# Kernel tuning notes

Measured on AMD Instinct MI355X. Metric: run time of the kernel, lower is better.

The kernel has to match this reference:

```python
import jax, jax.numpy as jnp
import numpy as np

C = 512
NUM_HEADS = 8
HEAD_DIM = C // NUM_HEADS


def setup_inputs() -> dict:
    key = jax.random.key(0)
    ks = jax.random.split(key, 5)
    B, H, W = 4, 48, 48
    x = jax.random.normal(ks[0], (B, C, H, W), dtype=jnp.float32)
    # 1x1 conv weights == dense matrices over channel dim
    Wqkv = jax.random.normal(ks[1], (3 * C, C), dtype=jnp.float32) * (1.0 / np.sqrt(C))
    bqkv = jax.random.normal(ks[2], (3 * C,), dtype=jnp.float32) * 0.01
    Wout = jax.random.normal(ks[3], (C, C), dtype=jnp.float32) * (1.0 / np.sqrt(C))
    bout = jax.random.normal(ks[4], (C,), dtype=jnp.float32) * 0.01
    return {"x": x, "Wqkv": Wqkv, "bqkv": bqkv, "Wout": Wout, "bout": bout}


def reference(x, Wqkv, bqkv, Wout, bout):
    B, Cc, H, W = x.shape
    S = H * W
    # qkv 1x1 conv: [B, 3C, H, W] -> reshape (B, 3, heads, head_dim, S)
    qkv = jnp.einsum('bchw,oc->bohw', x, Wqkv) + bqkv[None, :, None, None]
    qkv = qkv.reshape(B, 3, NUM_HEADS, HEAD_DIM, S)
    q, k, v = qkv[:, 0], qkv[:, 1], qkv[:, 2]  # [B, h, d, S]
    # tokens along S: q^T k, scaled softmax
    scale = HEAD_DIM ** -0.5
    attn = jnp.einsum('bhds,bhdt->bhst', q, k) * scale  # [B, h, S, S]
    attn = jax.nn.softmax(attn, axis=-1)
    out = jnp.einsum('bhst,bhdt->bhds', attn, v)  # [B, h, d, S]
    out = out.reshape(B, Cc, H, W)
    out = jnp.einsum('bchw,oc->bohw', out, Wout) + bout[None, :, None, None]
    return out
```

## Files before the change

kernel.cpp:

```cpp
#include <hip/hip_runtime.h>

#define S_LEN 2304
#define CDIM  512
#define NHEAD 8

typedef __attribute__((ext_vector_type(4)))  float f32x4;
typedef __attribute__((ext_vector_type(16))) float f32x16;
typedef __attribute__((ext_vector_type(8)))  _Float16 f16x8;
typedef __attribute__((ext_vector_type(2)))  __fp16 fp16x2r;
typedef _Float16 h16;

#define QSCALE 0.18033688011112042f

__device__ __forceinline__ float fexp2(float x) {
#if __has_builtin(__builtin_amdgcn_exp2f)
    return __builtin_amdgcn_exp2f(x);
#else
    return exp2f(x);
#endif
}

__device__ __forceinline__ unsigned cvtpk(float a, float b) {
    union { fp16x2r v; unsigned u; } c;
    c.v = __builtin_amdgcn_cvt_pkrtz(a, b);
    return c.u;
}

__device__ __forceinline__ void gll16(const h16* g, h16* l) {
    __builtin_amdgcn_global_load_lds(
        (const __attribute__((address_space(1))) unsigned int*)g,
        (__attribute__((address_space(3))) unsigned int*)l, 16, 0, 0);
}

__global__ __launch_bounds__(256) void xpose_x(
    const float* __restrict__ x, h16* __restrict__ xT)
{
    const int s0 = blockIdx.x * 64;
    const int c0 = blockIdx.y * 64;
    const int b  = blockIdx.z;
    __shared__ h16 Ts[64][76];

    const int t  = threadIdx.x;
    const int cq = t >> 4;
    const int sq = t & 15;

    const float* xb = x + ((size_t)b * CDIM + c0 + cq * 4) * S_LEN + s0 + sq * 4;
    float4 r0 = *(const float4*)(xb);
    float4 r1 = *(const float4*)(xb + S_LEN);
    float4 r2 = *(const float4*)(xb + 2 * S_LEN);
    float4 r3 = *(const float4*)(xb + 3 * S_LEN);

    union { h16 h[4]; uint2 u; } pk;
    pk.h[0]=(h16)r0.x; pk.h[1]=(h16)r1.x; pk.h[2]=(h16)r2.x; pk.h[3]=(h16)r3.x;
    *(uint2*)&Ts[sq*4+0][cq*4] = pk.u;
    pk.h[0]=(h16)r0.y; pk.h[1]=(h16)r1.y; pk.h[2]=(h16)r2.y; pk.h[3]=(h16)r3.y;
    *(uint2*)&Ts[sq*4+1][cq*4] = pk.u;
    pk.h[0]=(h16)r0.z; pk.h[1]=(h16)r1.z; pk.h[2]=(h16)r2.z; pk.h[3]=(h16)r3.z;
    *(uint2*)&Ts[sq*4+2][cq*4] = pk.u;
    pk.h[0]=(h16)r0.w; pk.h[1]=(h16)r1.w; pk.h[2]=(h16)r2.w; pk.h[3]=(h16)r3.w;
    *(uint2*)&Ts[sq*4+3][cq*4] = pk.u;

    __syncthreads();
    const int s  = t >> 2;
    const int cc = (t & 3) * 16;
    uint2 a0 = *(uint2*)&Ts[s][cc + 0];
    uint2 a1 = *(uint2*)&Ts[s][cc + 4];
    uint2 a2 = *(uint2*)&Ts[s][cc + 8];
    uint2 a3 = *(uint2*)&Ts[s][cc + 12];
    h16* dst = xT + ((size_t)b * S_LEN + s0 + s) * CDIM + c0 + cc;
    uint4 w0 = make_uint4(a0.x, a0.y, a1.x, a1.y);
    uint4 w1 = make_uint4(a2.x, a2.y, a3.x, a3.y);
    *(uint4*)dst       = w0;
    *(uint4*)(dst + 8) = w1;
}

__global__ __launch_bounds__(256) void wconv(
    const float* __restrict__ Wq, const float* __restrict__ Wo,
    h16* __restrict__ Wq_h, h16* __restrict__ Wo_h)
{
    const int NQ = 1536 * 512;
    const int NO = 512 * 512;
    int i = (blockIdx.x * 256 + threadIdx.x) * 4;
    if (i >= NQ + NO) return;
    float4 v;
    h16* dst;
    if (i < NQ) { v = *(const float4*)(Wq + i);        dst = Wq_h + i; }
    else        { v = *(const float4*)(Wo + (i - NQ)); dst = Wo_h + (i - NQ); }
    union { h16 h[4]; uint2 u; } pk;
    pk.h[0]=(h16)v.x; pk.h[1]=(h16)v.y; pk.h[2]=(h16)v.z; pk.h[3]=(h16)v.w;
    *(uint2*)dst = pk.u;
}

__global__ __launch_bounds__(256) void gemm_qkv(
    const h16* __restrict__ Wh, const float* __restrict__ bqkv,
    const h16* __restrict__ xT, h16* __restrict__ qT, h16* __restrict__ kT,
    h16* __restrict__ vN)
{
    const int n0 = blockIdx.x * 128;
    const int m0 = blockIdx.y * 128;
    const int b  = blockIdx.z;
    __shared__ h16 Ws[128 * 64];
    __shared__ h16 Xs[128 * 64];

    const int tid = threadIdx.x;
    const int lid = tid & 63, w = tid >> 6;
    const int g = lid >> 4, ln = lid & 15;
    const int wm = w & 1, wn = w >> 1;
    const int srow = lid >> 3;
    const int sblk = (lid & 7) ^ (srow & 7);

    f32x4 acc[4][4];
#pragma unroll
    for (int i = 0; i < 4; i++)
#pragma unroll
        for (int j = 0; j < 4; j++) acc[i][j] = (f32x4)0.f;

    const h16* Wbase = Wh + (size_t)m0 * CDIM;
    const h16* Xbase = xT + ((size_t)b * S_LEN + n0) * CDIM;
    const bool vblk = (m0 >= 1024);

    for (int kt = 0; kt < CDIM; kt += 64) {
        __syncthreads();
#pragma unroll
        for (int i = 0; i < 4; i++) {
            const int row0 = w * 32 + i * 8;
            gll16(Wbase + (size_t)(row0 + srow) * CDIM + kt + sblk * 8, &Ws[row0 * 64]);
            gll16(Xbase + (size_t)(row0 + srow) * CDIM + kt + sblk * 8, &Xs[row0 * 64]);
        }
        __syncthreads();

#pragma unroll
        for (int kc = 0; kc < 2; kc++) {
            f16x8 af[4], bf[4];
#pragma unroll
            for (int i = 0; i < 4; i++) {
                const int ra = wm * 64 + i * 16 + ln;
                const int ca = (kc * 64 + g * 16) ^ ((ra & 7) << 4);
                af[i] = *(const f16x8*)&Ws[ra * 64 + ca / 2];
                const int rb = wn * 64 + i * 16 + ln;
                const int cb = (kc * 64 + g * 16) ^ ((rb & 7) << 4);
                bf[i] = *(const f16x8*)&Xs[rb * 64 + cb / 2];
            }
            if (!vblk) {
#pragma unroll
                for (int i = 0; i < 4; i++)
#pragma unroll
                    for (int j = 0; j < 4; j++)
                        acc[i][j] = __builtin_amdgcn_mfma_f32_16x16x32_f16(
                            af[i], bf[j], acc[i][j], 0, 0, 0);
            } else {
#pragma unroll
                for (int i = 0; i < 4; i++)
#pragma unroll
                    for (int j = 0; j < 4; j++)
                        acc[i][j] = __builtin_amdgcn_mfma_f32_16x16x32_f16(
                            bf[i], af[j], acc[i][j], 0, 0, 0);
            }
        }
    }

    if (!vblk) {
#pragma unroll
        for (int i = 0; i < 4; i++) {
            const int mb = m0 + wm * 64 + i * 16 + 4 * g;
            const float4 bv = *(const float4*)&bqkv[mb];
            const int mloc = mb & 511;
            const int hh = mloc >> 6, d0 = mloc & 63;
            const bool isq = (mb < 512);
            const float scl = isq ? QSCALE : 1.0f;
            h16* base = (isq ? qT : kT);
#pragma unroll
            for (int j = 0; j < 4; j++) {
                const int n = n0 + wn * 64 + j * 16 + ln;
                union { h16 h[4]; uint2 u; } pk;
                pk.h[0] = (h16)((acc[i][j][0] + bv.x) * scl);
                pk.h[1] = (h16)((acc[i][j][1] + bv.y) * scl);
                pk.h[2] = (h16)((acc[i][j][2] + bv.z) * scl);
                pk.h[3] = (h16)((acc[i][j][3] + bv.w) * scl);
                *(uint2*)(base + (((size_t)b * 8 + hh) * S_LEN + n) * 64 + d0) = pk.u;
            }
        }
    } else {
#pragma unroll
        for (int j = 0; j < 4; j++) {
            const int m = m0 + wm * 64 + j * 16 + ln;
            const float bias = bqkv[m];
            const int mloc = m - 1024;
            const int hh = mloc >> 6, d = mloc & 63;
            h16* base = vN + (((size_t)b * 8 + hh) * 64 + d) * S_LEN;
#pragma unroll
            for (int i = 0; i < 4; i++) {
                const int nb = n0 + wn * 64 + i * 16 + 4 * g;
                union { h16 h[4]; uint2 u; } pk;
                pk.h[0] = (h16)(acc[i][j][0] + bias);
                pk.h[1] = (h16)(acc[i][j][1] + bias);
                pk.h[2] = (h16)(acc[i][j][2] + bias);
                pk.h[3] = (h16)(acc[i][j][3] + bias);
                *(uint2*)(base + nb) = pk.u;
            }
        }
    }
}

__global__ __launch_bounds__(192, 4) void attn_f16(
    const h16* __restrict__ qT, const h16* __restrict__ kT,
    const h16* __restrict__ vN, h16* __restrict__ attT)
{
    const int f    = blockIdx.x;
    const int xcd  = f & 7;
    const int slot = f >> 3;
    const int bh   = xcd + 8 * (slot / 24);
    const int x    = slot % 24;
    const int b    = bh >> 3;
    const int h    = bh & 7;
    const int s0   = x * 96;

    __shared__ h16 Ks[2][64 * 64];
    __shared__ h16 Vs[2][64 * 64];

    const int tid = threadIdx.x;
    const int lid = tid & 63, w = tid >> 6;
    const int l31 = lid & 31, hi = lid >> 5;
    const int srow = lid >> 3;
    const int sblk = (lid & 7) ^ (srow & 7);

    const h16* qb = qT + ((size_t)b * 8 + h) * S_LEN * 64;
    const h16* kb = kT + ((size_t)b * 8 + h) * S_LEN * 64;
    const h16* vb = vN + ((size_t)b * 8 + h) * 64 * S_LEN;

    const int sq = s0 + w * 32 + l31;

    f16x8 qf[4];
    {
        const h16* qrow = qb + (size_t)sq * 64;
#pragma unroll
        for (int ds = 0; ds < 4; ds++)
            qf[ds] = *(const f16x8*)(qrow + ds * 16 + hi * 8);
    }

    f16x8 ones;
#pragma unroll
    for (int i = 0; i < 8; i++) ones[i] = (h16)1.0f;

    for (int c = w; c < 16; c += 3) {
        if (c < 8)
            gll16(kb + (size_t)(c * 8 + srow) * 64 + sblk * 8, &Ks[0][c * 8 * 64]);
        else
            gll16(vb + (size_t)((c - 8) * 8 + srow) * S_LEN + sblk * 8,
                  &Vs[0][(c - 8) * 8 * 64]);
    }
    __syncthreads();

    float m_run = -1e30f;
    f32x16 oacc0 = (f32x16)0.f, oacc1 = (f32x16)0.f, lacc = (f32x16)0.f;

    int cur = 0;
    for (int kt = 0; kt < S_LEN; kt += 64, cur ^= 1) {
        if (kt + 64 < S_LEN) {
            for (int c = w; c < 16; c += 3) {
                if (c < 8)
                    gll16(kb + (size_t)(kt + 64 + c * 8 + srow) * 64 + sblk * 8,
                          &Ks[cur ^ 1][c * 8 * 64]);
                else
                    gll16(vb + (size_t)((c - 8) * 8 + srow) * S_LEN + kt + 64 + sblk * 8,
                          &Vs[cur ^ 1][(c - 8) * 8 * 64]);
            }
        }
        const h16* Kc = Ks[cur];
        const h16* Vc = Vs[cur];

        f32x16 sacc0 = (f32x16)0.f, sacc1 = (f32x16)0.f;
        __builtin_amdgcn_s_setprio(1);
#pragma unroll
        for (int ds = 0; ds < 4; ds++) {
            const int bc = 2 * ds + hi;
            {
                const int row = l31;
                f16x8 kf = *(const f16x8*)&Kc[row * 64 + ((bc ^ (row & 7)) * 8)];
                sacc0 = __builtin_amdgcn_mfma_f32_32x32x16_f16(kf, qf[ds], sacc0, 0, 0, 0);
            }
            {
                const int row = 32 + l31;
                f16x8 kf = *(const f16x8*)&Kc[row * 64 + ((bc ^ (row & 7)) * 8)];
                sacc1 = __builtin_amdgcn_mfma_f32_32x32x16_f16(kf, qf[ds], sacc1, 0, 0, 0);
            }
        }
        __builtin_amdgcn_s_setprio(0);

        float ma = sacc0[0], mb2 = sacc1[0];
#pragma unroll
        for (int r = 1; r < 15; r += 2) {
            ma  = fmaxf(fmaxf(ma,  sacc0[r]), sacc0[r + 1]);
            mb2 = fmaxf(fmaxf(mb2, sacc1[r]), sacc1[r + 1]);
        }
        ma  = fmaxf(ma,  sacc0[15]);
        mb2 = fmaxf(mb2, sacc1[15]);
        float mloc = fmaxf(ma, mb2);
        mloc = fmaxf(mloc, __shfl_xor(mloc, 32));

        if (!__all(mloc <= m_run + 8.0f)) {
            const float mnew = fmaxf(m_run, mloc);
            const float resc = fexp2(m_run - mnew);
#pragma unroll
            for (int r = 0; r < 16; r++) {
                oacc0[r] *= resc; oacc1[r] *= resc; lacc[r] *= resc;
            }
            m_run = mnew;
        }

#pragma unroll
        for (int r = 0; r < 16; r++) sacc0[r] = fexp2(sacc0[r] - m_run);
#pragma unroll
        for (int r = 0; r < 16; r++) sacc1[r] = fexp2(sacc1[r] - m_run);

        f16x8 pf[4];
#pragma unroll
        for (int i = 0; i < 4; i++) {
            const int bse = (i & 1) * 8;
            float pv[8];
#pragma unroll
            for (int r = 0; r < 8; r++)
                pv[r] = (i < 2) ? sacc0[bse + r] : sacc1[bse + r];
            unsigned X0 = cvtpk(pv[0], pv[1]);
            unsigned X1 = cvtpk(pv[2], pv[3]);
            unsigned Y0 = cvtpk(pv[4], pv[5]);
            unsigned Y1 = cvtpk(pv[6], pv[7]);
            asm("v_permlane32_swap_b32 %0, %1" : "+v"(X0), "+v"(Y0));
            asm("v_permlane32_swap_b32 %0, %1" : "+v"(X1), "+v"(Y1));
            union { unsigned u[4]; f16x8 v; } pkk;
            pkk.u[0] = X0; pkk.u[1] = X1; pkk.u[2] = Y0; pkk.u[3] = Y1;
            pf[i] = pkk.v;
        }

        __builtin_amdgcn_s_setprio(1);
#pragma unroll
        for (int i = 0; i < 4; i++) {
            const int bc = 2 * i + hi;
            lacc = __builtin_amdgcn_mfma_f32_32x32x16_f16(ones, pf[i], lacc, 0, 0, 0);
            {
                const int row = l31;
                f16x8 vf = *(const f16x8*)&Vc[row * 64 + ((bc ^ (row & 7)) * 8)];
                oacc0 = __builtin_amdgcn_mfma_f32_32x32x16_f16(vf, pf[i], oacc0, 0, 0, 0);
            }
            {
                const int row = 32 + l31;
                f16x8 vf = *(const f16x8*)&Vc[row * 64 + ((bc ^ (row & 7)) * 8)];
                oacc1 = __builtin_amdgcn_mfma_f32_32x32x16_f16(vf, pf[i], oacc1, 0, 0, 0);
            }
        }
        __builtin_amdgcn_s_setprio(0);
        __syncthreads();
    }

    const float inv = 1.0f / lacc[0];
    h16* ob = attT + ((size_t)b * S_LEN + sq) * CDIM + h * 64;
#pragma unroll
    for (int gi = 0; gi < 4; gi++) {
        union { h16 hh[4]; uint2 u; } p0, p1;
#pragma unroll
        for (int r = 0; r < 4; r++) {
            p0.hh[r] = (h16)(oacc0[gi * 4 + r] * inv);
            p1.hh[r] = (h16)(oacc1[gi * 4 + r] * inv);
        }
        *(uint2*)(ob + 8 * gi + 4 * hi)      = p0.u;
        *(uint2*)(ob + 32 + 8 * gi + 4 * hi) = p1.u;
    }
}

__global__ __launch_bounds__(256) void gemm_out(
    const h16* __restrict__ attT, const h16* __restrict__ Wh,
    const float* __restrict__ bout, float* __restrict__ out)
{
    const int n0 = blockIdx.x * 128;
    const int m0 = blockIdx.y * 128;
    const int b  = blockIdx.z;
    __shared__ h16 Ws[128 * 64];
    __shared__ h16 Xs[128 * 64];

    const int tid = threadIdx.x;
    const int lid = tid & 63, w = tid >> 6;
    const int g = lid >> 4, ln = lid & 15;
    const int wm = w & 1, wn = w >> 1;
    const int srow = lid >> 3;
    const int sblk = (lid & 7) ^ (srow & 7);

    f32x4 acc[4][4];
#pragma unroll
    for (int i = 0; i < 4; i++)
#pragma unroll
        for (int j = 0; j < 4; j++) acc[i][j] = (f32x4)0.f;

    const h16* Wbase = Wh + (size_t)m0 * CDIM;
    const h16* Xbase = attT + ((size_t)b * S_LEN + n0) * CDIM;

    for (int kt = 0; kt < CDIM; kt += 64) {
        __syncthreads();
#pragma unroll
        for (int i = 0; i < 4; i++) {
            const int row0 = w * 32 + i * 8;
            gll16(Wbase + (size_t)(row0 + srow) * CDIM + kt + sblk * 8, &Ws[row0 * 64]);
            gll16(Xbase + (size_t)(row0 + srow) * CDIM + kt + sblk * 8, &Xs[row0 * 64]);
        }
        __syncthreads();

#pragma unroll
        for (int kc = 0; kc < 2; kc++) {
            f16x8 af[4], bf[4];
#pragma unroll
            for (int i = 0; i < 4; i++) {
                const int ra = wm * 64 + i * 16 + ln;
                const int ca = (kc * 64 + g * 16) ^ ((ra & 7) << 4);
                af[i] = *(const f16x8*)&Ws[ra * 64 + ca / 2];
                const int rb = wn * 64 + i * 16 + ln;
                const int cb = (kc * 64 + g * 16) ^ ((rb & 7) << 4);
                bf[i] = *(const f16x8*)&Xs[rb * 64 + cb / 2];
            }
#pragma unroll
            for (int i = 0; i < 4; i++)
#pragma unroll
                for (int j = 0; j < 4; j++)
                    acc[i][j] = __builtin_amdgcn_mfma_f32_16x16x32_f16(
                        bf[i], af[j], acc[i][j], 0, 0, 0);
        }
    }

#pragma unroll
    for (int j = 0; j < 4; j++) {
        const int m = m0 + wm * 64 + j * 16 + ln;
        const float bias = bout[m];
        float* base = out + ((size_t)b * CDIM + m) * S_LEN;
#pragma unroll
        for (int i = 0; i < 4; i++) {
            const int nb = n0 + wn * 64 + i * 16 + 4 * g;
            float4 o;
            o.x = acc[i][j][0] + bias;
            o.y = acc[i][j][1] + bias;
            o.z = acc[i][j][2] + bias;
            o.w = acc[i][j][3] + bias;
            *(float4*)(base + nb) = o;
        }
    }
}

extern "C" void kernel_launch(void* const* d_in, const int* in_sizes, int n_in,
                              void* d_out, int out_size, void* d_ws, size_t ws_size,
                              hipStream_t stream)
{
    const float* x    = (const float*)d_in[0];
    const float* Wqkv = (const float*)d_in[1];
    const float* bqkv = (const float*)d_in[2];
    const float* Wout = (const float*)d_in[3];
    const float* bout = (const float*)d_in[4];
    float* out = (float*)d_out;

    h16* xT   = (h16*)d_ws;
    h16* Wq_h = xT   + (size_t)4 * S_LEN * CDIM;
    h16* Wo_h = Wq_h + (size_t)1536 * 512;
    h16* qT   = Wo_h + (size_t)512 * 512;
    h16* kT   = qT   + (size_t)4 * 8 * S_LEN * 64;
    h16* vN   = kT   + (size_t)4 * 8 * S_LEN * 64;
    h16* attT = vN   + (size_t)4 * 8 * S_LEN * 64;

    xpose_x <<<dim3(36, 8, 4),  256, 0, stream>>>(x, xT);
    wconv   <<<1024,            256, 0, stream>>>(Wqkv, Wout, Wq_h, Wo_h);
    gemm_qkv<<<dim3(18, 12, 4), 256, 0, stream>>>(Wq_h, bqkv, xT, qT, kT, vN);
    attn_f16<<<768,             192, 0, stream>>>(qT, kT, vN, attT);
    gemm_out<<<dim3(18, 4, 4),  256, 0, stream>>>(attT, Wo_h, bout, out);
}
```

Before: 136.6 us.

## Fuse prep kernels, software-pipeline attention PV step, halve output GEMM tile

Merges the x transpose and weight conversion into a single launch to save one kernel launch. The attention loop is restructured so the P·V product for the previous tile runs alongside the QK^T MFMAs of the current tile. V is now loaded in the same iteration it will be consumed in the next, and the synchronisation sits at the end of the loop. The output GEMM uses 64-wide N tiles to double the block count for better CU occupancy, at the cost of less reuse of each weight tile.

```diff
diff --git a/kernel.cpp b/kernel.cpp
--- a/kernel.cpp
+++ b/kernel.cpp
@@ -32,12 +32,29 @@
         (__attribute__((address_space(3))) unsigned int*)l, 16, 0, 0);
 }
 
-__global__ __launch_bounds__(256) void xpose_x(
-    const float* __restrict__ x, h16* __restrict__ xT)
+__global__ __launch_bounds__(256) void prep(
+    const float* __restrict__ x, h16* __restrict__ xT,
+    const float* __restrict__ Wq, const float* __restrict__ Wo,
+    h16* __restrict__ Wq_h, h16* __restrict__ Wo_h)
 {
-    const int s0 = blockIdx.x * 64;
-    const int c0 = blockIdx.y * 64;
-    const int b  = blockIdx.z;
+    const int bid = blockIdx.x;
+    if (bid >= 1152) {
+        const int NQ = 1536 * 512;
+        const int NO = 512 * 512;
+        int i = ((bid - 1152) * 256 + threadIdx.x) * 4;
+        if (i >= NQ + NO) return;
+        float4 v;
+        h16* dst;
+        if (i < NQ) { v = *(const float4*)(Wq + i);        dst = Wq_h + i; }
+        else        { v = *(const float4*)(Wo + (i - NQ)); dst = Wo_h + (i - NQ); }
+        union { h16 h[4]; uint2 u; } pk;
+        pk.h[0]=(h16)v.x; pk.h[1]=(h16)v.y; pk.h[2]=(h16)v.z; pk.h[3]=(h16)v.w;
+        *(uint2*)dst = pk.u;
+        return;
+    }
+    const int s0 = (bid % 36) * 64;
+    const int c0 = ((bid / 36) & 7) * 64;
+    const int b  = bid / 288;
     __shared__ h16 Ts[64][76];
 
     const int t  = threadIdx.x;
@@ -74,23 +91,6 @@
     *(uint4*)(dst + 8) = w1;
 }
 
-__global__ __launch_bounds__(256) void wconv(
-    const float* __restrict__ Wq, const float* __restrict__ Wo,
-    h16* __restrict__ Wq_h, h16* __restrict__ Wo_h)
-{
-    const int NQ = 1536 * 512;
-    const int NO = 512 * 512;
-    int i = (blockIdx.x * 256 + threadIdx.x) * 4;
-    if (i >= NQ + NO) return;
-    float4 v;
-    h16* dst;
-    if (i < NQ) { v = *(const float4*)(Wq + i);        dst = Wq_h + i; }
-    else        { v = *(const float4*)(Wo + (i - NQ)); dst = Wo_h + (i - NQ); }
-    union { h16 h[4]; uint2 u; } pk;
-    pk.h[0]=(h16)v.x; pk.h[1]=(h16)v.y; pk.h[2]=(h16)v.z; pk.h[3]=(h16)v.w;
-    *(uint2*)dst = pk.u;
-}
-
 __global__ __launch_bounds__(256) void gemm_qkv(
     const h16* __restrict__ Wh, const float* __restrict__ bqkv,
     const h16* __restrict__ xT, h16* __restrict__ qT, h16* __restrict__ kT,
@@ -242,32 +242,31 @@
 #pragma unroll
     for (int i = 0; i < 8; i++) ones[i] = (h16)1.0f;
 
-    for (int c = w; c < 16; c += 3) {
-        if (c < 8)
-            gll16(kb + (size_t)(c * 8 + srow) * 64 + sblk * 8, &Ks[0][c * 8 * 64]);
-        else
-            gll16(vb + (size_t)((c - 8) * 8 + srow) * S_LEN + sblk * 8,
-                  &Vs[0][(c - 8) * 8 * 64]);
-    }
+    for (int c = w; c < 8; c += 3)
+        gll16(kb + (size_t)(c * 8 + srow) * 64 + sblk * 8, &Ks[0][c * 8 * 64]);
     __syncthreads();
 
     float m_run = -1e30f;
     f32x16 oacc0 = (f32x16)0.f, oacc1 = (f32x16)0.f, lacc = (f32x16)0.f;
-
-    int cur = 0;
-    for (int kt = 0; kt < S_LEN; kt += 64, cur ^= 1) {
-        if (kt + 64 < S_LEN) {
-            for (int c = w; c < 16; c += 3) {
-                if (c < 8)
-                    gll16(kb + (size_t)(kt + 64 + c * 8 + srow) * 64 + sblk * 8,
-                          &Ks[cur ^ 1][c * 8 * 64]);
-                else
-                    gll16(vb + (size_t)((c - 8) * 8 + srow) * S_LEN + kt + 64 + sblk * 8,
-                          &Vs[cur ^ 1][(c - 8) * 8 * 64]);
-            }
-        }
-        const h16* Kc = Ks[cur];
-        const h16* Vc = Vs[cur];
+    f16x8 pf_prev[4];
+
+    const int NT = S_LEN / 64;
+    for (int i = 0; i < NT; i++) {
+        const int kcur = i & 1;
+        if (i + 1 < NT) {
+            const int kt1 = (i + 1) * 64;
+            for (int c = w; c < 8; c += 3)
+                gll16(kb + (size_t)(kt1 + c * 8 + srow) * 64 + sblk * 8,
+                      &Ks[kcur ^ 1][c * 8 * 64]);
+        }
+        {
+            const int kt0 = i * 64;
+            for (int c = w; c < 8; c += 3)
+                gll16(vb + (size_t)(c * 8 + srow) * S_LEN + kt0 + sblk * 8,
+                      &Vs[i & 1][c * 8 * 64]);
+        }
+
+        const h16* Kc = Ks[kcur];
 
         f32x16 sacc0 = (f32x16)0.f, sacc1 = (f32x16)0.f;
         __builtin_amdgcn_s_setprio(1);
@@ -285,6 +284,24 @@
                 sacc1 = __builtin_amdgcn_mfma_f32_32x32x16_f16(kf, qf[ds], sacc1, 0, 0, 0);
             }
         }
+        if (i > 0) {
+            const h16* Vp = Vs[(i - 1) & 1];
+#pragma unroll
+            for (int j = 0; j < 4; j++) {
+                const int bc = 2 * j + hi;
+                lacc = __builtin_amdgcn_mfma_f32_32x32x16_f16(ones, pf_prev[j], lacc, 0, 0, 0);
+                {
+                    const int row = l31;
+                    f16x8 vf = *(const f16x8*)&Vp[row * 64 + ((bc ^ (row & 7)) * 8)];
+                    oacc0 = __builtin_amdgcn_mfma_f32_32x32x16_f16(vf, pf_prev[j], oacc0, 0, 0, 0);
+                }
+                {
+                    const int row = 32 + l31;
+                    f16x8 vf = *(const f16x8*)&Vp[row * 64 + ((bc ^ (row & 7)) * 8)];
+                    oacc1 = __builtin_amdgcn_mfma_f32_32x32x16_f16(vf, pf_prev[j], oacc1, 0, 0, 0);
+                }
+            }
+        }
         __builtin_amdgcn_s_setprio(0);
 
         float ma = sacc0[0], mb2 = sacc1[0];
@@ -313,14 +330,13 @@
 #pragma unroll
         for (int r = 0; r < 16; r++) sacc1[r] = fexp2(sacc1[r] - m_run);
 
-        f16x8 pf[4];
-#pragma unroll
-        for (int i = 0; i < 4; i++) {
-            const int bse = (i & 1) * 8;
+#pragma unroll
+        for (int j = 0; j < 4; j++) {
+            const int bse = (j & 1) * 8;
             float pv[8];
 #pragma unroll
             for (int r = 0; r < 8; r++)
-                pv[r] = (i < 2) ? sacc0[bse + r] : sacc1[bse + r];
+                pv[r] = (j < 2) ? sacc0[bse + r] : sacc1[bse + r];
             unsigned X0 = cvtpk(pv[0], pv[1]);
             unsigned X1 = cvtpk(pv[2], pv[3]);
             unsigned Y0 = cvtpk(pv[4], pv[5]);
@@ -329,27 +345,28 @@
             asm("v_permlane32_swap_b32 %0, %1" : "+v"(X1), "+v"(Y1));
             union { unsigned u[4]; f16x8 v; } pkk;
             pkk.u[0] = X0; pkk.u[1] = X1; pkk.u[2] = Y0; pkk.u[3] = Y1;
-            pf[i] = pkk.v;
-        }
-
-        __builtin_amdgcn_s_setprio(1);
-#pragma unroll
-        for (int i = 0; i < 4; i++) {
-            const int bc = 2 * i + hi;
-            lacc = __builtin_amdgcn_mfma_f32_32x32x16_f16(ones, pf[i], lacc, 0, 0, 0);
+            pf_prev[j] = pkk.v;
+        }
+        __syncthreads();
+    }
+
+    {
+        const h16* Vp = Vs[(NT - 1) & 1];
+#pragma unroll
+        for (int j = 0; j < 4; j++) {
+            const int bc = 2 * j + hi;
+            lacc = __builtin_amdgcn_mfma_f32_32x32x16_f16(ones, pf_prev[j], lacc, 0, 0, 0);
             {
                 const int row = l31;
-                f16x8 vf = *(const f16x8*)&Vc[row * 64 + ((bc ^ (row & 7)) * 8)];
-                oacc0 = __builtin_amdgcn_mfma_f32_32x32x16_f16(vf, pf[i], oacc0, 0, 0, 0);
+                f16x8 vf = *(const f16x8*)&Vp[row * 64 + ((bc ^ (row & 7)) * 8)];
+                oacc0 = __builtin_amdgcn_mfma_f32_32x32x16_f16(vf, pf_prev[j], oacc0, 0, 0, 0);
             }
             {
                 const int row = 32 + l31;
-                f16x8 vf = *(const f16x8*)&Vc[row * 64 + ((bc ^ (row & 7)) * 8)];
-                oacc1 = __builtin_amdgcn_mfma_f32_32x32x16_f16(vf, pf[i], oacc1, 0, 0, 0);
-            }
-        }
-        __builtin_amdgcn_s_setprio(0);
-        __syncthreads();
+                f16x8 vf = *(const f16x8*)&Vp[row * 64 + ((bc ^ (row & 7)) * 8)];
+                oacc1 = __builtin_amdgcn_mfma_f32_32x32x16_f16(vf, pf_prev[j], oacc1, 0, 0, 0);
+            }
+        }
     }
 
     const float inv = 1.0f / lacc[0];
@@ -371,11 +388,11 @@
     const h16* __restrict__ attT, const h16* __restrict__ Wh,
     const float* __restrict__ bout, float* __restrict__ out)
 {
-    const int n0 = blockIdx.x * 128;
+    const int n0 = blockIdx.x * 64;
     const int m0 = blockIdx.y * 128;
     const int b  = blockIdx.z;
     __shared__ h16 Ws[128 * 64];
-    __shared__ h16 Xs[128 * 64];
+    __shared__ h16 Xs[64 * 64];
 
     const int tid = threadIdx.x;
     const int lid = tid & 63, w = tid >> 6;
@@ -384,9 +401,9 @@
     const int srow = lid >> 3;
     const int sblk = (lid & 7) ^ (srow & 7);
 
-    f32x4 acc[4][4];
-#pragma unroll
-    for (int i = 0; i < 4; i++)
+    f32x4 acc[2][4];
+#pragma unroll
+    for (int i = 0; i < 2; i++)
 #pragma unroll
         for (int j = 0; j < 4; j++) acc[i][j] = (f32x4)0.f;
 
@@ -399,24 +416,32 @@
         for (int i = 0; i < 4; i++) {
             const int row0 = w * 32 + i * 8;
             gll16(Wbase + (size_t)(row0 + srow) * CDIM + kt + sblk * 8, &Ws[row0 * 64]);
-            gll16(Xbase + (size_t)(row0 + srow) * CDIM + kt + sblk * 8, &Xs[row0 * 64]);
+        }
+#pragma unroll
+        for (int i = 0; i < 2; i++) {
+            const int row0 = w * 16 + i * 8;
+            if (row0 < 64)
+                gll16(Xbase + (size_t)(row0 + srow) * CDIM + kt + sblk * 8, &Xs[row0 * 64]);
         }
         __syncthreads();
 
 #pragma unroll
         for (int kc = 0; kc < 2; kc++) {
-            f16x8 af[4], bf[4];
-#pragma unroll
-            for (int i = 0; i < 4; i++) {
-                const int ra = wm * 64 + i * 16 + ln;
+            f16x8 af[4], bf[2];
+#pragma unroll
+            for (int j = 0; j < 4; j++) {
+                const int ra = wm * 64 + j * 16 + ln;
                 const int ca = (kc * 64 + g * 16) ^ ((ra & 7) << 4);
-                af[i] = *(const f16x8*)&Ws[ra * 64 + ca / 2];
-                const int rb = wn * 64 + i * 16 + ln;
+                af[j] = *(const f16x8*)&Ws[ra * 64 + ca / 2];
+            }
+#pragma unroll
+            for (int i = 0; i < 2; i++) {
+                const int rb = wn * 32 + i * 16 + ln;
                 const int cb = (kc * 64 + g * 16) ^ ((rb & 7) << 4);
                 bf[i] = *(const f16x8*)&Xs[rb * 64 + cb / 2];
             }
 #pragma unroll
-            for (int i = 0; i < 4; i++)
+            for (int i = 0; i < 2; i++)
 #pragma unroll
                 for (int j = 0; j < 4; j++)
                     acc[i][j] = __builtin_amdgcn_mfma_f32_16x16x32_f16(
@@ -430,8 +455,8 @@
         const float bias = bout[m];
         float* base = out + ((size_t)b * CDIM + m) * S_LEN;
 #pragma unroll
-        for (int i = 0; i < 4; i++) {
-            const int nb = n0 + wn * 64 + i * 16 + 4 * g;
+        for (int i = 0; i < 2; i++) {
+            const int nb = n0 + wn * 32 + i * 16 + 4 * g;
             float4 o;
             o.x = acc[i][j][0] + bias;
             o.y = acc[i][j][1] + bias;
@@ -461,9 +486,8 @@
     h16* vN   = kT   + (size_t)4 * 8 * S_LEN * 64;
     h16* attT = vN   + (size_t)4 * 8 * S_LEN * 64;
 
-    xpose_x <<<dim3(36, 8, 4),  256, 0, stream>>>(x, xT);
-    wconv   <<<1024,            256, 0, stream>>>(Wqkv, Wout, Wq_h, Wo_h);
+    prep    <<<2176,            256, 0, stream>>>(x, xT, Wqkv, Wout, Wq_h, Wo_h);
     gemm_qkv<<<dim3(18, 12, 4), 256, 0, stream>>>(Wq_h, bqkv, xT, qT, kT, vN);
     attn_f16<<<768,             192, 0, stream>>>(qT, kT, vN, attT);
-    gemm_out<<<dim3(18, 4, 4),  256, 0, stream>>>(attT, Wo_h, bout, out);
-}
+    gemm_out<<<dim3(36, 4, 4),  256, 0, stream>>>(attT, Wo_h, bout, out);
+}
```

Result: no change. 136.4 us (-0.1%).
